# Optimization experiments

Measured on AMD Instinct MI355X. Metric: run time of the kernel, lower is better.

The kernel has to match this reference:

```python
import jax, jax.numpy as jnp
import numpy as np
import math

NUM_HEADS = 8
HIDDEN = 128  # per-head dim == model dim (residual stream)
B, S = 4, 2048
LN_EPS = 1e-6
NEG = -1e9


def setup_inputs() -> dict:
    key = jax.random.key(0)
    ks = jax.random.split(key, 7)
    enc = jax.random.normal(ks[0], (B, S, HIDDEN), dtype=jnp.float32)
    mask = jax.random.randint(ks[1], (B, 1, S, S), 0, 2, dtype=jnp.int32)
    sc = 1.0 / math.sqrt(HIDDEN)
    Wq = jax.random.normal(ks[2], (HIDDEN, HIDDEN * NUM_HEADS), dtype=jnp.float32) * sc
    Wk = jax.random.normal(ks[3], (HIDDEN, HIDDEN * NUM_HEADS), dtype=jnp.float32) * sc
    Wv = jax.random.normal(ks[4], (HIDDEN, HIDDEN * NUM_HEADS), dtype=jnp.float32) * sc
    Wo = jax.random.normal(ks[5], (HIDDEN * NUM_HEADS, HIDDEN), dtype=jnp.float32) * sc
    ln_scale = jnp.ones((HIDDEN,), dtype=jnp.float32)
    ln_bias = jnp.zeros((HIDDEN,), dtype=jnp.float32)
    return {"enc": enc, "mask": mask, "Wq": Wq, "Wk": Wk, "Wv": Wv,
            "Wo": Wo, "ln_scale": ln_scale, "ln_bias": ln_bias}


def _layer_norm(x, scale, bias):
    mu = jnp.mean(x, axis=-1, keepdims=True)
    var = jnp.mean(jnp.square(x - mu), axis=-1, keepdims=True)
    return (x - mu) * jax.lax.rsqrt(var + LN_EPS) * scale + bias


def reference(enc, mask, Wq, Wk, Wv, Wo, ln_scale, ln_bias):
    b, s, d = enc.shape
    h = Wq.shape[1] // d
    # projections -> [b, h, s, d]
    def proj(W):
        return jnp.einsum('bsd,de->bse', enc, W).reshape(b, s, h, d).transpose(0, 2, 1, 3)
    Q, K, V = proj(Wq), proj(Wk), proj(Wv)
    scores = jnp.einsum('bhqd,bhkd->bhqk', Q, K) / math.sqrt(d)
    scores = jnp.where(mask == 0, jnp.float32(NEG), scores)
    attn = jax.nn.softmax(scores, axis=-1)  # dropout is identity in eval mode
    out = jnp.einsum('bhqk,bhkd->bhqd', attn, V)
    out = out.transpose(0, 2, 1, 3).reshape(b, s, h * d)
    out = jnp.einsum('bse,ed->bsd', out, Wo)
    out = _layer_norm(out + enc, ln_scale, ln_bias)
    return (out, attn)
```

## Files before the change

### kernel.cpp

```cpp
#include <hip/hip_runtime.h>
#include <hip/hip_bf16.h>
#include <cstdint>
#include <cstddef>

typedef __bf16 bf16;
typedef __bf16 bf16x8 __attribute__((ext_vector_type(8)));
typedef float  f32x4  __attribute__((ext_vector_type(4)));
typedef unsigned int uint32;

#define MFMA16(a, b, c) __builtin_amdgcn_mfma_f32_16x16x32_bf16((a), (b), (c), 0, 0, 0)

static constexpr int Bn = 4, Hn = 8, Sn = 2048, Dn = 128, En = 1024;


__global__ void k_cvt_enc(const float* __restrict__ in, bf16* __restrict__ out) {
    int i = blockIdx.x * 256 + threadIdx.x;
    out[i] = (bf16)in[i];
}

__global__ void k_cvt_w(const float* __restrict__ w, bf16* __restrict__ wt,
                        int dinLog, int doutLog, float scale) {
    int idx = blockIdx.x * 256 + threadIdx.x;
    int n = idx >> dinLog;
    int k = idx & ((1 << dinLog) - 1);
    wt[idx] = (bf16)(w[(k << doutLog) + n] * scale);
}

__global__ void k_bitmask(const int* __restrict__ m, uint32* __restrict__ bits) {
    int idx = blockIdx.x * 256 + threadIdx.x;
    unsigned long long b = __ballot(m[idx] != 0);
    if ((threadIdx.x & 63) == 0) {
        bits[(idx >> 5)]     = (uint32)b;
        bits[(idx >> 5) + 1] = (uint32)(b >> 32);
    }
}


__global__ __launch_bounds__(256) void k_proj(const bf16* __restrict__ encB,
                                              const bf16* __restrict__ wT0,
                                              const bf16* __restrict__ wT1,
                                              const bf16* __restrict__ wT2,
                                              bf16* __restrict__ qb,
                                              bf16* __restrict__ kbuf,
                                              bf16* __restrict__ vt) {
    const int tid = threadIdx.x, w = tid >> 6, lane = tid & 63;
    const int quad = lane >> 4, l15 = lane & 15;
    const int mat = blockIdx.z;
    const int hh  = blockIdx.y;
    const int e0  = hh * 128;
    const int row0 = blockIdx.x * 64 + w * 16;
    const bf16* wT = (mat == 0) ? wT0 : ((mat == 1) ? wT1 : wT2);

    bf16x8 a[4];
#pragma unroll
    for (int kc = 0; kc < 4; kc++)
        a[kc] = *(const bf16x8*)(encB + (row0 + l15) * Dn + kc * 32 + quad * 8);

    f32x4 acc[8];
#pragma unroll
    for (int nt = 0; nt < 8; nt++) { f32x4 z = {0.f, 0.f, 0.f, 0.f}; acc[nt] = z; }

#pragma unroll
    for (int kc = 0; kc < 4; kc++) {
#pragma unroll
        for (int nt = 0; nt < 8; nt++) {
            bf16x8 b = *(const bf16x8*)(wT + (e0 + nt * 16 + l15) * Dn + kc * 32 + quad * 8);
            acc[nt] = MFMA16(a[kc], b, acc[nt]);
        }
    }

    __shared__ bf16 tile[4 * 16 * 128];
#pragma unroll
    for (int nt = 0; nt < 8; nt++)
#pragma unroll
        for (int r = 0; r < 4; r++)
            tile[(w * 16 + quad * 4 + r) * 128 + nt * 16 + l15] = (bf16)acc[nt][r];
    __syncthreads();

    if (mat < 2) {
        bf16* outp = (mat == 0) ? qb : kbuf;
#pragma unroll
        for (int it = 0; it < 4; it++) {
            int rr = it * 4 + quad;
            int s  = blockIdx.x * 64 + w * 16 + rr;
            int bb = s >> 11, sl = s & 2047;
            bf16* dst = outp + (((size_t)(bb * Hn + hh) * Sn + sl) * Dn) + l15 * 8;
            *(uint4*)dst = *(const uint4*)(tile + (w * 16 + rr) * 128 + l15 * 8);
        }
    } else {
        int dr  = tid >> 1;
        int sc0 = (tid & 1) * 32;
        int sg  = blockIdx.x * 64;
        int bb  = sg >> 11, sl0 = sg & 2047;
        unsigned short tmp[32];
#pragma unroll
        for (int i = 0; i < 32; i++) {
            int sl = sc0 + i;
            tmp[i] = *(const unsigned short*)(tile + sl * 128 + dr);
        }
        bf16* dst = vt + ((size_t)(bb * Hn + hh) * Dn + dr) * Sn + sl0 + sc0;
#pragma unroll
        for (int i = 0; i < 4; i++)
            *(uint4*)(dst + i * 8) = *(const uint4*)(tmp + i * 8);
    }
}


__global__ __launch_bounds__(256, 2) void k_attn(const bf16* __restrict__ qb,
                                                 const bf16* __restrict__ kbuf,
                                                 const bf16* __restrict__ vt,
                                                 const uint32* __restrict__ bits,
                                                 float* __restrict__ attn,
                                                 bf16* __restrict__ ob) {
    const int tid = threadIdx.x, w = tid >> 6, lane = tid & 63;
    const int quad = lane >> 4, l15 = lane & 15;
    const int qblk = blockIdx.x;
    const int bh   = blockIdx.y;
    const int bb   = bh >> 3, hh = bh & 7;
    const int qw0  = qblk * 128 + w * 32;

    __shared__ __align__(16) char smem[56320];
    bf16*  Klds = (bf16*)smem;
    bf16*  Vlds = (bf16*)(smem + 17408);
    float* Plds = (float*)(smem + 37888);
    float* Pw   = Plds + w * (32 * 36);

    const bf16* Kbase = kbuf + (size_t)bh * Sn * Dn;
    const bf16* Qbase = qb   + (size_t)bh * Sn * Dn;
    const bf16* Vbase = vt   + (size_t)bh * Dn * Sn;
    const uint32* mbase = bits + (size_t)bb * (Sn * (Sn / 32));
    float* attnbase = attn + (size_t)bh * Sn * Sn;

    bf16x8 aq[2][4];
#pragma unroll
    for (int qs = 0; qs < 2; qs++)
#pragma unroll
        for (int kc = 0; kc < 4; kc++)
            aq[qs][kc] = *(const bf16x8*)(Qbase + (qw0 + qs * 16 + l15) * Dn + kc * 32 + quad * 8);

    float lsum[8];
#pragma unroll
    for (int ri = 0; ri < 8; ri++) lsum[ri] = 0.f;

    for (int kb = 0; kb < Sn / 64; kb++) {
        {
            int krow = tid >> 2, c0 = (tid & 3) * 32;
            const bf16* src = Kbase + (size_t)(kb * 64 + krow) * Dn + c0;
            bf16* dst = Klds + krow * 136 + c0;
#pragma unroll
            for (int i = 0; i < 4; i++)
                *(uint4*)(dst + i * 8) = *(const uint4*)(src + i * 8);
        }
        __syncthreads();

        uint32 mw0[8], mw1[8];
#pragma unroll
        for (int ri = 0; ri < 8; ri++) {
            int q = qw0 + (ri >> 2) * 16 + quad * 4 + (ri & 3);
            mw0[ri] = mbase[q * (Sn / 32) + kb * 2];
            mw1[ri] = mbase[q * (Sn / 32) + kb * 2 + 1];
        }

#pragma unroll
        for (int ct = 0; ct < 4; ct++) {
            f32x4 z = {0.f, 0.f, 0.f, 0.f};
            f32x4 sc0 = z, sc1 = z;
#pragma unroll
            for (int kc = 0; kc < 4; kc++) {
                bf16x8 bk = *(const bf16x8*)(Klds + (ct * 16 + l15) * 136 + kc * 32 + quad * 8);
                sc0 = MFMA16(aq[0][kc], bk, sc0);
                sc1 = MFMA16(aq[1][kc], bk, sc1);
            }
            int sh = (ct & 1) * 16 + l15;
            int hi = ct >> 1;
#pragma unroll
            for (int r = 0; r < 4; r++) {
                uint32 m0 = hi ? mw1[r] : mw0[r];
                float v0 = ((m0 >> sh) & 1u) ? sc0[r] : -1e9f;
                lsum[r] += __expf(v0);
                uint32 m1 = hi ? mw1[4 + r] : mw0[4 + r];
                float v1 = ((m1 >> sh) & 1u) ? sc1[r] : -1e9f;
                lsum[4 + r] += __expf(v1);
            }
        }
        __syncthreads();
    }

    float invl[8];
#pragma unroll
    for (int ri = 0; ri < 8; ri++) {
        float t = lsum[ri];
        t += __shfl_xor(t, 1, 64);
        t += __shfl_xor(t, 2, 64);
        t += __shfl_xor(t, 4, 64);
        t += __shfl_xor(t, 8, 64);
        invl[ri] = (t > 0.f) ? (1.0f / t) : 0.0f;
    }

    f32x4 o[2][8];
#pragma unroll
    for (int qs = 0; qs < 2; qs++)
#pragma unroll
        for (int nt = 0; nt < 8; nt++) { f32x4 z = {0.f, 0.f, 0.f, 0.f}; o[qs][nt] = z; }

    for (int kb = 0; kb < Sn / 64; kb++) {
        {
            int krow = tid >> 2, c0 = (tid & 3) * 32;
            const bf16* src = Kbase + (size_t)(kb * 64 + krow) * Dn + c0;
            bf16* dst = Klds + krow * 136 + c0;
#pragma unroll
            for (int i = 0; i < 4; i++)
                *(uint4*)(dst + i * 8) = *(const uint4*)(src + i * 8);
        }
        {
            int dr = tid >> 1, c0 = (tid & 1) * 32;
            const bf16* src = Vbase + (size_t)dr * Sn + kb * 64 + c0;
            bf16* dst = Vlds + dr * 80 + c0;
#pragma unroll
            for (int i = 0; i < 4; i++)
                *(uint4*)(dst + i * 8) = *(const uint4*)(src + i * 8);
        }
        __syncthreads();

        uint32 mw0[8], mw1[8];
#pragma unroll
        for (int ri = 0; ri < 8; ri++) {
            int q = qw0 + (ri >> 2) * 16 + quad * 4 + (ri & 3);
            mw0[ri] = mbase[q * (Sn / 32) + kb * 2];
            mw1[ri] = mbase[q * (Sn / 32) + kb * 2 + 1];
        }

#pragma unroll
        for (int kt = 0; kt < 2; kt++) {
            f32x4 sc[2][2];
#pragma unroll
            for (int ct2 = 0; ct2 < 2; ct2++) {
                f32x4 z = {0.f, 0.f, 0.f, 0.f};
                sc[ct2][0] = z; sc[ct2][1] = z;
                int ct = kt * 2 + ct2;
#pragma unroll
                for (int kc = 0; kc < 4; kc++) {
                    bf16x8 bk = *(const bf16x8*)(Klds + (ct * 16 + l15) * 136 + kc * 32 + quad * 8);
                    sc[ct2][0] = MFMA16(aq[0][kc], bk, sc[ct2][0]);
                    sc[ct2][1] = MFMA16(aq[1][kc], bk, sc[ct2][1]);
                }
            }
#pragma unroll
            for (int ct2 = 0; ct2 < 2; ct2++) {
                int ct = kt * 2 + ct2;
                int sh = (ct & 1) * 16 + l15;
                int hi = ct >> 1;
#pragma unroll
                for (int qs = 0; qs < 2; qs++)
#pragma unroll
                    for (int r = 0; r < 4; r++) {
                        uint32 mwrd = hi ? mw1[qs * 4 + r] : mw0[qs * 4 + r];
                        float v = ((mwrd >> sh) & 1u) ? sc[ct2][qs][r] : -1e9f;
                        float il = invl[qs * 4 + r];
                        float p = __expf(v) * il + ((il == 0.f) ? (1.0f / 2048.0f) : 0.f);
                        int q = qw0 + qs * 16 + quad * 4 + r;
                        attnbase[(size_t)q * Sn + kb * 64 + kt * 32 + ct2 * 16 + l15] = p;
                        Pw[(qs * 16 + quad * 4 + r) * 36 + ct2 * 16 + l15] = p;
                    }
            }
            bf16x8 ap[2];
#pragma unroll
            for (int qs = 0; qs < 2; qs++) {
                f32x4 p0 = *(const f32x4*)(Pw + (qs * 16 + l15) * 36 + quad * 8);
                f32x4 p1 = *(const f32x4*)(Pw + (qs * 16 + l15) * 36 + quad * 8 + 4);
                bf16x8 t;
                t[0] = (bf16)p0[0]; t[1] = (bf16)p0[1]; t[2] = (bf16)p0[2]; t[3] = (bf16)p0[3];
                t[4] = (bf16)p1[0]; t[5] = (bf16)p1[1]; t[6] = (bf16)p1[2]; t[7] = (bf16)p1[3];
                ap[qs] = t;
            }
#pragma unroll
            for (int nt = 0; nt < 8; nt++) {
                bf16x8 bv = *(const bf16x8*)(Vlds + (nt * 16 + l15) * 80 + kt * 32 + quad * 8);
                o[0][nt] = MFMA16(ap[0], bv, o[0][nt]);
                o[1][nt] = MFMA16(ap[1], bv, o[1][nt]);
            }
        }
        __syncthreads();
    }

    bf16* Olds = (bf16*)smem;
    bf16* Ow = Olds + w * (32 * 128);
#pragma unroll
    for (int qs = 0; qs < 2; qs++)
#pragma unroll
        for (int nt = 0; nt < 8; nt++)
#pragma unroll
            for (int r = 0; r < 4; r++)
                Ow[(qs * 16 + quad * 4 + r) * 128 + nt * 16 + l15] = (bf16)o[qs][nt][r];
#pragma unroll
    for (int it = 0; it < 8; it++) {
        int rr = it * 4 + quad;
        int s = qblk * 128 + w * 32 + rr;
        bf16* dst = ob + ((size_t)bb * Sn + s) * En + hh * Dn + l15 * 8;
        *(uint4*)dst = *(const uint4*)(Ow + rr * 128 + l15 * 8);
    }
}


__global__ __launch_bounds__(256) void k_final(const bf16* __restrict__ ob,
                                               const bf16* __restrict__ woT,
                                               const float* __restrict__ enc,
                                               const float* __restrict__ lnsc,
                                               const float* __restrict__ lnbi,
                                               float* __restrict__ out) {
    const int tid = threadIdx.x, w = tid >> 6, lane = tid & 63;
    const int quad = lane >> 4, l15 = lane & 15;
    const int row0 = blockIdx.x * 64 + w * 16;

    f32x4 acc[8];
#pragma unroll
    for (int nt = 0; nt < 8; nt++) { f32x4 z = {0.f, 0.f, 0.f, 0.f}; acc[nt] = z; }

    for (int kc = 0; kc < 32; kc++) {
        bf16x8 a = *(const bf16x8*)(ob + (size_t)(row0 + l15) * En + kc * 32 + quad * 8);
#pragma unroll
        for (int nt = 0; nt < 8; nt++) {
            bf16x8 b = *(const bf16x8*)(woT + (size_t)(nt * 16 + l15) * En + kc * 32 + quad * 8);
            acc[nt] = MFMA16(a, b, acc[nt]);
        }
    }

#pragma unroll
    for (int r = 0; r < 4; r++) {
        int row = row0 + quad * 4 + r;
        float xv[8];
        float s1 = 0.f, s2 = 0.f;
#pragma unroll
        for (int nt = 0; nt < 8; nt++) {
            float xx = acc[nt][r] + enc[(size_t)row * Dn + nt * 16 + l15];
            xv[nt] = xx;
            s1 += xx;
            s2 += xx * xx;
        }
        s1 += __shfl_xor(s1, 1, 64); s2 += __shfl_xor(s2, 1, 64);
        s1 += __shfl_xor(s1, 2, 64); s2 += __shfl_xor(s2, 2, 64);
        s1 += __shfl_xor(s1, 4, 64); s2 += __shfl_xor(s2, 4, 64);
        s1 += __shfl_xor(s1, 8, 64); s2 += __shfl_xor(s2, 8, 64);
        float mu = s1 * (1.0f / 128.0f);
        float var = s2 * (1.0f / 128.0f) - mu * mu;
        float rs = rsqrtf(var + 1e-6f);
#pragma unroll
        for (int nt = 0; nt < 8; nt++) {
            int col = nt * 16 + l15;
            out[(size_t)row * Dn + col] = (xv[nt] - mu) * rs * lnsc[col] + lnbi[col];
        }
    }
}


extern "C" void kernel_launch(void* const* d_in, const int* in_sizes, int n_in,
                              void* d_out, int out_size, void* d_ws, size_t ws_size,
                              hipStream_t stream) {
    (void)in_sizes; (void)n_in; (void)out_size; (void)ws_size;
    const float* enc  = (const float*)d_in[0];
    const int*   mask = (const int*)d_in[1];
    const float* Wq   = (const float*)d_in[2];
    const float* Wk   = (const float*)d_in[3];
    const float* Wv   = (const float*)d_in[4];
    const float* Wo   = (const float*)d_in[5];
    const float* lnsc = (const float*)d_in[6];
    const float* lnbi = (const float*)d_in[7];

    char* ws = (char*)d_ws;
    bf16*   encB = (bf16*)(ws + 0);
    bf16*   WqT  = (bf16*)(ws + 2097152);
    bf16*   WkT  = (bf16*)(ws + 2359296);
    bf16*   WvT  = (bf16*)(ws + 2621440);
    bf16*   WoT  = (bf16*)(ws + 2883584);
    uint32* bits = (uint32*)(ws + 3145728);
    bf16*   QB   = (bf16*)(ws + 5242880);
    bf16*   KB   = (bf16*)(ws + 22020096);
    bf16*   VT   = (bf16*)(ws + 38797312);
    bf16*   OB   = (bf16*)(ws + 55574528);

    float* outp = (float*)d_out;
    float* attn = outp + (size_t)Bn * Sn * Dn;

    k_cvt_enc<<<dim3(4096), dim3(256), 0, stream>>>(enc, encB);
    k_cvt_w<<<dim3(512), dim3(256), 0, stream>>>(Wq, WqT, 7, 10, 0.08838834764831845f);
    k_cvt_w<<<dim3(512), dim3(256), 0, stream>>>(Wk, WkT, 7, 10, 1.0f);
    k_cvt_w<<<dim3(512), dim3(256), 0, stream>>>(Wv, WvT, 7, 10, 1.0f);
    k_cvt_w<<<dim3(512), dim3(256), 0, stream>>>(Wo, WoT, 10, 7, 1.0f);
    k_bitmask<<<dim3(65536), dim3(256), 0, stream>>>(mask, bits);
    k_proj<<<dim3(128, 8, 3), dim3(256), 0, stream>>>(encB, WqT, WkT, WvT, QB, KB, VT);
    k_attn<<<dim3(16, 32), dim3(256), 0, stream>>>(QB, KB, VT, bits, attn, OB);
    k_final<<<dim3(128), dim3(256), 0, stream>>>(OB, WoT, enc, lnsc, lnbi, outp);
}
```

Before: 957.2 us.

## Vectorize attn stores via LDS transpose, pad V tile, widen mask loads, set MFMA priority

The attention-probability output is now written to global memory as 16-byte vector stores, using rows read back from the per-wave LDS P tile, instead of scalar strided 4-byte stores. The V LDS row stride is padded from 80 to 88 to reduce bank conflicts, mask words are loaded as uint2, and s_setprio raises wave priority around MFMA blocks. The main target is the write bandwidth of the large fp32 attn tensor. In exchange, LDS use grows slightly and register live ranges change.

```diff
diff --git a/kernel.cpp b/kernel.cpp
--- a/kernel.cpp
+++ b/kernel.cpp
@@ -119,10 +119,10 @@
     const int bb   = bh >> 3, hh = bh & 7;
     const int qw0  = qblk * 128 + w * 32;
 
-    __shared__ __align__(16) char smem[56320];
+    __shared__ __align__(16) char smem[58368];
     bf16*  Klds = (bf16*)smem;
     bf16*  Vlds = (bf16*)(smem + 17408);
-    float* Plds = (float*)(smem + 37888);
+    float* Plds = (float*)(smem + 39936);
     float* Pw   = Plds + w * (32 * 36);
 
     const bf16* Kbase = kbuf + (size_t)bh * Sn * Dn;
@@ -157,20 +157,22 @@
 #pragma unroll
         for (int ri = 0; ri < 8; ri++) {
             int q = qw0 + (ri >> 2) * 16 + quad * 4 + (ri & 3);
-            mw0[ri] = mbase[q * (Sn / 32) + kb * 2];
-            mw1[ri] = mbase[q * (Sn / 32) + kb * 2 + 1];
+            uint2 m = *(const uint2*)(mbase + (size_t)q * (Sn / 32) + kb * 2);
+            mw0[ri] = m.x; mw1[ri] = m.y;
         }
 
 #pragma unroll
         for (int ct = 0; ct < 4; ct++) {
             f32x4 z = {0.f, 0.f, 0.f, 0.f};
             f32x4 sc0 = z, sc1 = z;
+            __builtin_amdgcn_s_setprio(1);
 #pragma unroll
             for (int kc = 0; kc < 4; kc++) {
                 bf16x8 bk = *(const bf16x8*)(Klds + (ct * 16 + l15) * 136 + kc * 32 + quad * 8);
                 sc0 = MFMA16(aq[0][kc], bk, sc0);
                 sc1 = MFMA16(aq[1][kc], bk, sc1);
             }
+            __builtin_amdgcn_s_setprio(0);
             int sh = (ct & 1) * 16 + l15;
             int hi = ct >> 1;
 #pragma unroll
@@ -215,7 +217,7 @@
         {
             int dr = tid >> 1, c0 = (tid & 1) * 32;
             const bf16* src = Vbase + (size_t)dr * Sn + kb * 64 + c0;
-            bf16* dst = Vlds + dr * 80 + c0;
+            bf16* dst = Vlds + dr * 88 + c0;
 #pragma unroll
             for (int i = 0; i < 4; i++)
                 *(uint4*)(dst + i * 8) = *(const uint4*)(src + i * 8);
@@ -226,59 +228,66 @@
 #pragma unroll
         for (int ri = 0; ri < 8; ri++) {
             int q = qw0 + (ri >> 2) * 16 + quad * 4 + (ri & 3);
-            mw0[ri] = mbase[q * (Sn / 32) + kb * 2];
-            mw1[ri] = mbase[q * (Sn / 32) + kb * 2 + 1];
+            uint2 m = *(const uint2*)(mbase + (size_t)q * (Sn / 32) + kb * 2);
+            mw0[ri] = m.x; mw1[ri] = m.y;
         }
 
 #pragma unroll
         for (int kt = 0; kt < 2; kt++) {
-            f32x4 sc[2][2];
 #pragma unroll
             for (int ct2 = 0; ct2 < 2; ct2++) {
+                int ct = kt * 2 + ct2;
                 f32x4 z = {0.f, 0.f, 0.f, 0.f};
-                sc[ct2][0] = z; sc[ct2][1] = z;
-                int ct = kt * 2 + ct2;
+                f32x4 s0 = z, s1 = z;
+                __builtin_amdgcn_s_setprio(1);
 #pragma unroll
                 for (int kc = 0; kc < 4; kc++) {
                     bf16x8 bk = *(const bf16x8*)(Klds + (ct * 16 + l15) * 136 + kc * 32 + quad * 8);
-                    sc[ct2][0] = MFMA16(aq[0][kc], bk, sc[ct2][0]);
-                    sc[ct2][1] = MFMA16(aq[1][kc], bk, sc[ct2][1]);
+                    s0 = MFMA16(aq[0][kc], bk, s0);
+                    s1 = MFMA16(aq[1][kc], bk, s1);
                 }
-            }
-#pragma unroll
-            for (int ct2 = 0; ct2 < 2; ct2++) {
-                int ct = kt * 2 + ct2;
+                __builtin_amdgcn_s_setprio(0);
                 int sh = (ct & 1) * 16 + l15;
                 int hi = ct >> 1;
 #pragma unroll
-                for (int qs = 0; qs < 2; qs++)
-#pragma unroll
-                    for (int r = 0; r < 4; r++) {
-                        uint32 mwrd = hi ? mw1[qs * 4 + r] : mw0[qs * 4 + r];
-                        float v = ((mwrd >> sh) & 1u) ? sc[ct2][qs][r] : -1e9f;
-                        float il = invl[qs * 4 + r];
+                for (int r = 0; r < 4; r++) {
+                    {
+                        uint32 m = hi ? mw1[r] : mw0[r];
+                        float v = ((m >> sh) & 1u) ? s0[r] : -1e9f;
+                        float il = invl[r];
                         float p = __expf(v) * il + ((il == 0.f) ? (1.0f / 2048.0f) : 0.f);
-                        int q = qw0 + qs * 16 + quad * 4 + r;
-                        attnbase[(size_t)q * Sn + kb * 64 + kt * 32 + ct2 * 16 + l15] = p;
-                        Pw[(qs * 16 + quad * 4 + r) * 36 + ct2 * 16 + l15] = p;
+                        Pw[(quad * 4 + r) * 36 + ct2 * 16 + l15] = p;
                     }
+                    {
+                        uint32 m = hi ? mw1[4 + r] : mw0[4 + r];
+                        float v = ((m >> sh) & 1u) ? s1[r] : -1e9f;
+                        float il = invl[4 + r];
+                        float p = __expf(v) * il + ((il == 0.f) ? (1.0f / 2048.0f) : 0.f);
+                        Pw[(16 + quad * 4 + r) * 36 + ct2 * 16 + l15] = p;
+                    }
+                }
             }
             bf16x8 ap[2];
 #pragma unroll
             for (int qs = 0; qs < 2; qs++) {
                 f32x4 p0 = *(const f32x4*)(Pw + (qs * 16 + l15) * 36 + quad * 8);
                 f32x4 p1 = *(const f32x4*)(Pw + (qs * 16 + l15) * 36 + quad * 8 + 4);
+                float* gd = attnbase + (size_t)(qw0 + qs * 16 + l15) * Sn + kb * 64 + kt * 32 + quad * 8;
+                *(f32x4*)gd = p0;
+                *(f32x4*)(gd + 4) = p1;
                 bf16x8 t;
                 t[0] = (bf16)p0[0]; t[1] = (bf16)p0[1]; t[2] = (bf16)p0[2]; t[3] = (bf16)p0[3];
                 t[4] = (bf16)p1[0]; t[5] = (bf16)p1[1]; t[6] = (bf16)p1[2]; t[7] = (bf16)p1[3];
                 ap[qs] = t;
             }
+            __builtin_amdgcn_s_setprio(1);
 #pragma unroll
             for (int nt = 0; nt < 8; nt++) {
-                bf16x8 bv = *(const bf16x8*)(Vlds + (nt * 16 + l15) * 80 + kt * 32 + quad * 8);
+                bf16x8 bv = *(const bf16x8*)(Vlds + (nt * 16 + l15) * 88 + kt * 32 + quad * 8);
                 o[0][nt] = MFMA16(ap[0], bv, o[0][nt]);
                 o[1][nt] = MFMA16(ap[1], bv, o[1][nt]);
             }
+            __builtin_amdgcn_s_setprio(0);
         }
         __syncthreads();
     }
```

Result: faster. 898.4 us (-6.1%).
